# Kernel tuning notes

Measured on AMD Instinct MI355X. Metric: run time of the kernel, lower is better.

## Reference

```python
import jax, jax.numpy as jnp
import numpy as np

# Production-scale dims (see shape_source)
N = 100_000      # total nodes (tokens)
E = 1_600_000    # edges
B = 2_000        # graphs / documents
VOCAB = 50_000
NW = 256         # word_vec width == GraphConv out channels (args.nw)
ENC = 512        # args.enc_nh
K = 100          # args.num_topic
EPS = 1e-5       # BatchNorm eps


def setup_inputs() -> dict:
    key = jax.random.key(0)
    ks = jax.random.split(key, 24)
    idx_x = jax.random.randint(ks[0], (N,), 0, VOCAB)
    idx_w = jnp.ones((1,), jnp.float32)          # scalar self-loop weight
    x_batch = jnp.sort(jax.random.randint(ks[1], (N,), 0, B))
    edge_index = jax.random.randint(ks[2], (2, E), 0, N)
    edge_weight = jax.random.uniform(ks[3], (E,), jnp.float32)
    # Parameters
    s = 0.02
    word_vec = jax.random.normal(ks[4], (VOCAB, NW), jnp.float32) * s
    Wrel = jax.random.normal(ks[5], (NW, NW), jnp.float32) * s   # GraphConv lin_rel
    brel = jnp.zeros((NW,), jnp.float32)
    Wroot = jax.random.normal(ks[6], (NW, NW), jnp.float32) * s  # GraphConv lin_root (no bias)
    bn_gamma = jnp.ones((NW,), jnp.float32)
    bn_beta = jnp.zeros((NW,), jnp.float32)
    W1 = jax.random.normal(ks[7], (ENC, 2 * NW), jnp.float32) * s  # enc2_fc1
    b1 = jnp.zeros((ENC,), jnp.float32)
    W2 = jax.random.normal(ks[8], (ENC, 2 * NW), jnp.float32) * s  # enc2_fc2
    b2 = jnp.zeros((ENC,), jnp.float32)
    Wm = jax.random.normal(ks[9], (K, ENC), jnp.float32) * s       # mean_fc
    bm = jnp.zeros((K,), jnp.float32)
    Wv = jnp.zeros((K, ENC), jnp.float32)                          # logvar_fc zero-init
    bv = jnp.zeros((K,), jnp.float32)
    Wphi = jax.random.normal(ks[10], (K, 2 * NW + ENC), jnp.float32) * s  # phi_fc
    bphi = jnp.zeros((K,), jnp.float32)
    return dict(idx_x=idx_x, idx_w=idx_w, x_batch=x_batch, edge_index=edge_index,
                edge_weight=edge_weight, word_vec=word_vec, Wrel=Wrel, brel=brel,
                Wroot=Wroot, bn_gamma=bn_gamma, bn_beta=bn_beta, W1=W1, b1=b1,
                W2=W2, b2=b2, Wm=Wm, bm=bm, Wv=Wv, bv=bv, Wphi=Wphi, bphi=bphi)


def reference(idx_x, idx_w, x_batch, edge_index, edge_weight, word_vec,
              Wrel, brel, Wroot, bn_gamma, bn_beta, W1, b1, W2, b2,
              Wm, bm, Wv, bv, Wphi, bphi):
    # Embedding gather
    x = word_vec[idx_x]                                # [N, NW]
    src, dst = edge_index[0], edge_index[1]
    # GraphConv with explicit self-loops of weight idx_w (diag edges in original)
    msg = edge_weight[:, None] * x[src]                # [E, NW]
    aggr = jax.ops.segment_sum(msg, dst, num_segments=N) + idx_w * x
    h = aggr @ Wrel.T + brel + x @ Wroot.T             # lin_rel(aggr) + lin_root(x)
    # BatchNorm1d (training-mode batch stats, biased variance) + tanh
    mu = jnp.mean(h, axis=0)
    var = jnp.mean((h - mu) ** 2, axis=0)
    enc1 = jnp.tanh((h - mu) * jax.lax.rsqrt(var + EPS) * bn_gamma + bn_beta)
    enc1 = jnp.concatenate([enc1, x], axis=-1)         # [N, 2*NW]
    # GLU gate
    enc2 = jax.nn.sigmoid(enc1 @ W1.T + b1) * jnp.tanh(enc1 @ W2.T + b2)  # [N, ENC]
    # Scatter-sum pooling per document (dropout is identity in eval)
    pooled = jax.ops.segment_sum(enc2, x_batch, num_segments=B)            # [B, ENC]
    mean = pooled @ Wm.T + bm                          # [B, K]
    logvar = pooled @ Wv.T + bv                        # [B, K]
    # Gather re-expansion + softmax
    word_embed = jnp.concatenate([enc1, pooled[x_batch]], axis=-1)         # [N, 2*NW+ENC]
    phi = jax.nn.softmax(word_embed @ Wphi.T + bphi, axis=-1)              # [N, K]
    return mean, logvar, phi
```

## Files before the change

kernel.cpp:

```cpp
#include <hip/hip_runtime.h>
#include <hip/hip_bf16.h>

#define NW 256
#define D2 512
#define PK 1024
#define BM 128
#define BK 64
#define DPB 8

typedef unsigned short u16;
typedef short bf16x8 __attribute__((ext_vector_type(8)));
typedef float f32x4 __attribute__((ext_vector_type(4)));

__device__ __forceinline__ float bf2f(u16 u) {
    union { unsigned u; float f; } v; v.u = ((unsigned)u) << 16; return v.f;
}
__device__ __forceinline__ u16 f2bf(float f) {
    union { float f; unsigned u; } v; v.f = f;
    unsigned u = v.u;
    return (u16)((u + 0x7fffu + ((u >> 16) & 1u)) >> 16);
}
__device__ __forceinline__ float tanh_fast(float x) {
    return 1.f - 2.f / (1.f + __expf(2.f * x));
}

__device__ __forceinline__ void stage_tile(const u16* __restrict__ base, int row0, int maxrow,
                                           int ldk, int k0, u16* lds, int tid) {
    int w = tid >> 6, l = tid & 63;
#pragma unroll
    for (int i = 0; i < 4; ++i) {
        int loadIdx = i * 256 + w * 64 + l;
        int row = loadIdx >> 3, s = loadIdx & 7;
        int srow = row0 + row; if (srow > maxrow) srow = maxrow;
        int scol = k0 + ((s ^ (row & 7)) << 3);
        const u16* g = base + (size_t)srow * ldk + scol;
        u16* ld = lds + (size_t)(i * 256 + w * 64) * 8;
        __builtin_amdgcn_global_load_lds((const __attribute__((address_space(1))) void*)g,
                                         (__attribute__((address_space(3))) void*)ld, 16, 0, 0);
    }
}

__device__ __forceinline__ bf16x8 lds_frag(const u16* lds, int row, int kc, int g) {
    int byte = (row << 7) + (kc << 6) + (g << 4);
    byte ^= (row & 7) << 4;
    return *(const bf16x8*)((const char*)lds + byte);
}

__global__ void k_wcat(const float* __restrict__ Wrel, const float* __restrict__ Wroot,
                       u16* __restrict__ wcat) {
    int i = blockIdx.x * blockDim.x + threadIdx.x;
    if (i < NW * D2) {
        int c = i >> 9, k = i & 511;
        float v = (k < NW) ? Wrel[c * NW + k] : Wroot[c * NW + (k - NW)];
        wcat[i] = f2bf(v);
    }
}
__global__ void k_wpair(const float* __restrict__ W1, const float* __restrict__ W2,
                        u16* __restrict__ wp) {
    int i = blockIdx.x * blockDim.x + threadIdx.x;
    if (i < 1024 * 512) {
        int row = i >> 9, k = i & 511;
        int c = row >> 7, j = row & 127;
        float v = (j < 64) ? W1[(size_t)(c * 64 + j) * D2 + k]
                           : W2[(size_t)(c * 64 + j - 64) * D2 + k];
        wp[i] = f2bf(v);
    }
}
__global__ void k_wphi(const float* __restrict__ Wphi, u16* __restrict__ wp, int K) {
    int i = blockIdx.x * blockDim.x + threadIdx.x;
    if (i < 128 * 1024) {
        int r = i >> 10, k = i & 1023;
        wp[i] = f2bf(r < K ? Wphi[(size_t)r * PK + k] : 0.f);
    }
}

__global__ void k_gather(const int* __restrict__ idx, const float* __restrict__ wv,
                         u16* __restrict__ X, int N) {
    int row = blockIdx.x * 4 + (threadIdx.x >> 6);
    int lane = threadIdx.x & 63;
    if (row < N) {
        int id = idx[row];
        float4 v = *(const float4*)(wv + (size_t)id * NW + lane * 4);
        ushort4 o;
        o.x = f2bf(v.x); o.y = f2bf(v.y); o.z = f2bf(v.z); o.w = f2bf(v.w);
        *(ushort4*)(X + (size_t)row * D2 + NW + lane * 4) = o;
    }
}

__global__ void k_hist(const int* __restrict__ ei, int* __restrict__ deg, int E) {
    int e = blockIdx.x * blockDim.x + threadIdx.x;
    if (e < E) atomicAdd(&deg[ei[E + e]], 1);
}
__global__ __launch_bounds__(1024) void k_scan(const int* __restrict__ deg,
                                               int* __restrict__ rowptr, int N) {
    const int T = 1024;
    int t = threadIdx.x;
    int chunk = (N + T - 1) / T;
    int beg = t * chunk, end = min(beg + chunk, N);
    int s = 0;
    for (int i = beg; i < end; ++i) s += deg[i];
    __shared__ int ls[T];
    ls[t] = s; __syncthreads();
    for (int d = 1; d < T; d <<= 1) {
        int v = (t >= d) ? ls[t - d] : 0;
        __syncthreads();
        ls[t] += v;
        __syncthreads();
    }
    int run = ls[t] - s;
    for (int i = beg; i < end; ++i) { rowptr[i] = run; run += deg[i]; }
    if (t == T - 1) rowptr[N] = run;
}
__global__ void k_scatter(const int* __restrict__ ei, const float* __restrict__ ew,
                          const int* __restrict__ rowptr, int* __restrict__ cursor,
                          int* __restrict__ ecols, float* __restrict__ evals, int E) {
    int e = blockIdx.x * blockDim.x + threadIdx.x;
    if (e < E) {
        int d = ei[E + e];
        int p = rowptr[d] + atomicAdd(&cursor[d], 1);
        ecols[p] = ei[e];
        evals[p] = ew[e];
    }
}

__global__ void k_spmm(const int* __restrict__ rowptr, const int* __restrict__ ecols,
                       const float* __restrict__ evals, const float* __restrict__ idxw,
                       u16* __restrict__ X, int N) {
    int n = blockIdx.x * 4 + (threadIdx.x >> 6);
    int l = threadIdx.x & 63;
    if (n >= N) return;
    int half = l >> 5, li = l & 31;
    float a[8];
    bf16x8 xv = *(const bf16x8*)(X + (size_t)n * D2 + NW + li * 8);
    float iw = idxw[0];
#pragma unroll
    for (int j = 0; j < 8; ++j) a[j] = half ? 0.f : iw * bf2f((u16)xv[j]);
    int r0 = rowptr[n], r1 = rowptr[n + 1];
#pragma unroll 4
    for (int e = r0 + half; e < r1; e += 2) {
        int s = ecols[e];
        float w = evals[e];
        bf16x8 v = *(const bf16x8*)(X + (size_t)s * D2 + NW + li * 8);
#pragma unroll
        for (int j = 0; j < 8; ++j) a[j] += w * bf2f((u16)v[j]);
    }
#pragma unroll
    for (int j = 0; j < 8; ++j) a[j] += __shfl_xor(a[j], 32);
    if (half == 0) {
        bf16x8 o;
#pragma unroll
        for (int j = 0; j < 8; ++j) o[j] = (short)f2bf(a[j]);
        *(bf16x8*)(X + (size_t)n * D2 + li * 8) = o;
    }
}

__global__ __launch_bounds__(256) void k_gemm_h(const u16* __restrict__ A, const u16* __restrict__ W,
                                                const float* __restrict__ brel, u16* __restrict__ H,
                                                float* __restrict__ sums, float* __restrict__ sumsq,
                                                int M, int MT) {
    int b = blockIdx.x;
    int xcd = b & 7, j = b >> 3;
    int chunk = j & 1;
    int panel = (j >> 1) * 8 + xcd;
    if (panel >= MT) return;
    __shared__ u16 As[2][BM * BK], Ws[2][BM * BK];
    int tid = threadIdx.x;
    int w = tid >> 6, l = tid & 63, l16 = l & 15, g = l >> 4;
    int row0 = panel * BM;
    const u16* wbase = W + (size_t)chunk * 128 * D2;
    f32x4 acc[2][8];
#pragma unroll
    for (int m = 0; m < 2; ++m)
#pragma unroll
        for (int n = 0; n < 8; ++n) { f32x4 z = {0.f, 0.f, 0.f, 0.f}; acc[m][n] = z; }

    stage_tile(A, row0, M - 1, D2, 0, As[0], tid);
    stage_tile(wbase, 0, 127, D2, 0, Ws[0], tid);
    __syncthreads();
    int buf = 0;
    for (int kt = 0; kt < 8; ++kt) {
        if (kt < 7) {
            stage_tile(A, row0, M - 1, D2, (kt + 1) * BK, As[buf ^ 1], tid);
            stage_tile(wbase, 0, 127, D2, (kt + 1) * BK, Ws[buf ^ 1], tid);
        }
#pragma unroll
        for (int kc = 0; kc < 2; ++kc) {
            bf16x8 a0 = lds_frag(As[buf], w * 32 + l16, kc, g);
            bf16x8 a1 = lds_frag(As[buf], w * 32 + 16 + l16, kc, g);
#pragma unroll
            for (int n = 0; n < 8; ++n) {
                bf16x8 bb = lds_frag(Ws[buf], n * 16 + l16, kc, g);
                acc[0][n] = __builtin_amdgcn_mfma_f32_16x16x32_bf16(a0, bb, acc[0][n], 0, 0, 0);
                acc[1][n] = __builtin_amdgcn_mfma_f32_16x16x32_bf16(a1, bb, acc[1][n], 0, 0, 0);
            }
        }
        __syncthreads();
        buf ^= 1;
    }
    float* ssum = (float*)As[0];
    float* ssq  = ssum + 128;
    if (tid < 128) { ssum[tid] = 0.f; ssq[tid] = 0.f; }
    __syncthreads();
    int colb = chunk * 128;
#pragma unroll
    for (int n = 0; n < 8; ++n) {
        int lcol = n * 16 + l16;
        int col = colb + lcol;
        float bb = brel[col];
        float cs = 0.f, cq = 0.f;
#pragma unroll
        for (int m = 0; m < 2; ++m) {
            int row = row0 + w * 32 + m * 16 + g * 4;
#pragma unroll
            for (int r = 0; r < 4; ++r) {
                if (row + r < M) {
                    float v = acc[m][n][r] + bb;
                    H[(size_t)(row + r) * NW + col] = f2bf(v);
                    cs += v; cq += v * v;
                }
            }
        }
        cs += __shfl_xor(cs, 16); cs += __shfl_xor(cs, 32);
        cq += __shfl_xor(cq, 16); cq += __shfl_xor(cq, 32);
        if (g == 0) { atomicAdd(&ssum[lcol], cs); atomicAdd(&ssq[lcol], cq); }
    }
    __syncthreads();
    if (tid < 128) {
        atomicAdd(&sums[colb + tid], ssum[tid]);
        atomicAdd(&sumsq[colb + tid], ssq[tid]);
    }
}

__global__ void k_bnprep(const float* __restrict__ sums, const float* __restrict__ sumsq,
                         const float* __restrict__ gamma, const float* __restrict__ beta,
                         float* __restrict__ bnab, int N) {
    int c = threadIdx.x;
    float inv = 1.f / (float)N;
    float mu = sums[c] * inv;
    float var = sumsq[c] * inv - mu * mu;
    float rs = rsqrtf(var + 1e-5f);
    float a = rs * gamma[c];
    bnab[c] = a;
    bnab[NW + c] = beta[c] - mu * a;
}

__global__ void k_enc1(const u16* __restrict__ H, const float* __restrict__ bnab,
                       u16* __restrict__ X, int N) {
    int row = blockIdx.x * 4 + (threadIdx.x >> 6);
    int lane = threadIdx.x & 63;
    if (row >= N) return;
    int c = lane * 4;
    ushort4 hv = *(const ushort4*)(H + (size_t)row * NW + c);
    ushort4 o;
    o.x = f2bf(tanh_fast(bf2f(hv.x) * bnab[c + 0] + bnab[NW + c + 0]));
    o.y = f2bf(tanh_fast(bf2f(hv.y) * bnab[c + 1] + bnab[NW + c + 1]));
    o.z = f2bf(tanh_fast(bf2f(hv.z) * bnab[c + 2] + bnab[NW + c + 2]));
    o.w = f2bf(tanh_fast(bf2f(hv.w) * bnab[c + 3] + bnab[NW + c + 3]));
    *(ushort4*)(X + (size_t)row * D2 + c) = o;
}

__global__ __launch_bounds__(256) void k_glu(const u16* __restrict__ A, const u16* __restrict__ Wp,
                                             const float* __restrict__ b1, const float* __restrict__ b2,
                                             u16* __restrict__ enc2, int M, int MT) {
    int b = blockIdx.x;
    int xcd = b & 7, j = b >> 3;
    int chunk = j & 7;
    int panel = (j >> 3) * 8 + xcd;
    if (panel >= MT) return;
    __shared__ u16 As[2][BM * BK], Ws[2][BM * BK];
    int tid = threadIdx.x;
    int w = tid >> 6, l = tid & 63, l16 = l & 15, g = l >> 4;
    int row0 = panel * BM;
    const u16* wbase = Wp + (size_t)chunk * 128 * D2;
    f32x4 acc[2][8];
#pragma unroll
    for (int m = 0; m < 2; ++m)
#pragma unroll
        for (int n = 0; n < 8; ++n) { f32x4 z = {0.f, 0.f, 0.f, 0.f}; acc[m][n] = z; }

    stage_tile(A, row0, M - 1, D2, 0, As[0], tid);
    stage_tile(wbase, 0, 127, D2, 0, Ws[0], tid);
    __syncthreads();
    int buf = 0;
    for (int kt = 0; kt < 8; ++kt) {
        if (kt < 7) {
            stage_tile(A, row0, M - 1, D2, (kt + 1) * BK, As[buf ^ 1], tid);
            stage_tile(wbase, 0, 127, D2, (kt + 1) * BK, Ws[buf ^ 1], tid);
        }
#pragma unroll
        for (int kc = 0; kc < 2; ++kc) {
            bf16x8 a0 = lds_frag(As[buf], w * 32 + l16, kc, g);
            bf16x8 a1 = lds_frag(As[buf], w * 32 + 16 + l16, kc, g);
#pragma unroll
            for (int n = 0; n < 8; ++n) {
                bf16x8 bb = lds_frag(Ws[buf], n * 16 + l16, kc, g);
                acc[0][n] = __builtin_amdgcn_mfma_f32_16x16x32_bf16(a0, bb, acc[0][n], 0, 0, 0);
                acc[1][n] = __builtin_amdgcn_mfma_f32_16x16x32_bf16(a1, bb, acc[1][n], 0, 0, 0);
            }
        }
        __syncthreads();
        buf ^= 1;
    }
    int colb = chunk * 64;
#pragma unroll
    for (int m = 0; m < 2; ++m) {
        int row = row0 + w * 32 + m * 16 + g * 4;
#pragma unroll
        for (int n = 0; n < 4; ++n) {
            int col = colb + n * 16 + l16;
            float f1 = b1[col], f2 = b2[col];
#pragma unroll
            for (int r = 0; r < 4; ++r) {
                if (row + r < M) {
                    float g1 = acc[m][n][r] + f1;
                    float g2 = acc[m][n + 4][r] + f2;
                    float sg = 1.f / (1.f + __expf(-g1));
                    enc2[(size_t)(row + r) * D2 + col] = f2bf(sg * tanh_fast(g2));
                }
            }
        }
    }
}

__global__ void k_docptr(const int* __restrict__ xb, int* __restrict__ dp, int N, int B) {
    int b = blockIdx.x * blockDim.x + threadIdx.x;
    if (b <= B) {
        int lo = 0, hi = N;
        while (lo < hi) { int mid = (lo + hi) >> 1; if (xb[mid] < b) lo = mid + 1; else hi = mid; }
        dp[b] = lo;
    }
}

__global__ void k_pool(const u16* __restrict__ enc2, const int* __restrict__ dp,
                       float* __restrict__ pooled, u16* __restrict__ pooledb, int B) {
    int b = blockIdx.x, t = threadIdx.x;
    int r0 = dp[b], r1 = dp[b + 1];
    float a0 = 0.f, a1 = 0.f;
    for (int r = r0; r < r1; ++r) {
        a0 += bf2f(enc2[(size_t)r * D2 + t]);
        a1 += bf2f(enc2[(size_t)r * D2 + 256 + t]);
    }
    pooled[(size_t)b * D2 + t] = a0;
    pooled[(size_t)b * D2 + 256 + t] = a1;
    pooledb[(size_t)b * D2 + t] = f2bf(a0);
    pooledb[(size_t)b * D2 + 256 + t] = f2bf(a1);
}

__global__ __launch_bounds__(128) void k_meanvar(const float* __restrict__ pooled,
                                                 const float* __restrict__ Wm,
                                                 const float* __restrict__ bm,
                                                 const float* __restrict__ Wv,
                                                 const float* __restrict__ bv,
                                                 float* __restrict__ out, int B, int K) {
    __shared__ float sp[DPB][D2];
    int b0 = blockIdx.x * DPB;
    int t = threadIdx.x;
    for (int i = t; i < DPB * D2; i += 128) {
        int d = i >> 9, c = i & 511;
        int b = b0 + d;
        sp[d][c] = (b < B) ? pooled[(size_t)b * D2 + c] : 0.f;
    }
    __syncthreads();
    if (t < K) {
        float m[DPB], v[DPB];
#pragma unroll
        for (int d = 0; d < DPB; ++d) { m[d] = 0.f; v[d] = 0.f; }
        const float* wm = Wm + (size_t)t * D2;
        const float* wv = Wv + (size_t)t * D2;
        for (int c = 0; c < D2; ++c) {
            float a = wm[c], bb = wv[c];
#pragma unroll
            for (int d = 0; d < DPB; ++d) {
                m[d] += sp[d][c] * a;
                v[d] += sp[d][c] * bb;
            }
        }
        float mb = bm[t], vb = bv[t];
#pragma unroll
        for (int d = 0; d < DPB; ++d) {
            int b = b0 + d;
            if (b < B) {
                out[(size_t)b * K + t] = m[d] + mb;
                out[(size_t)B * K + (size_t)b * K + t] = v[d] + vb;
            }
        }
    }
}

__device__ __forceinline__ void stage_phiA(const u16* __restrict__ X, const u16* __restrict__ PB,
                                           const int* __restrict__ xb, int row0, int M,
                                           int k0, u16* lds, int tid) {
    int w = tid >> 6, l = tid & 63;
#pragma unroll
    for (int i = 0; i < 4; ++i) {
        int loadIdx = i * 256 + w * 64 + l;
        int row = loadIdx >> 3, s = loadIdx & 7;
        int srow = row0 + row; if (srow >= M) srow = M - 1;
        int scol = k0 + ((s ^ (row & 7)) << 3);
        const u16* gsrc = (scol < D2) ? X + (size_t)srow * D2 + scol
                                      : PB + (size_t)xb[srow] * D2 + (scol - D2);
        u16* ld = lds + (size_t)(i * 256 + w * 64) * 8;
        __builtin_amdgcn_global_load_lds((const __attribute__((address_space(1))) void*)gsrc,
                                         (__attribute__((address_space(3))) void*)ld, 16, 0, 0);
    }
}

__global__ __launch_bounds__(256) void k_phi(const u16* __restrict__ X, const u16* __restrict__ PB,
                                             const int* __restrict__ xb, const u16* __restrict__ Wp,
                                             const float* __restrict__ bphi, float* __restrict__ out,
                                             int M, int B, int K) {
    __shared__ u16 As[2][BM * BK], Ws[2][BM * BK];
    int tid = threadIdx.x;
    int w = tid >> 6, l = tid & 63, l16 = l & 15, g = l >> 4;
    int row0 = blockIdx.x * BM;
    f32x4 acc[2][8];
#pragma unroll
    for (int m = 0; m < 2; ++m)
#pragma unroll
        for (int n = 0; n < 8; ++n) { f32x4 z = {0.f, 0.f, 0.f, 0.f}; acc[m][n] = z; }

    stage_phiA(X, PB, xb, row0, M, 0, As[0], tid);
    stage_tile(Wp, 0, 127, PK, 0, Ws[0], tid);
    __syncthreads();
    int buf = 0;
    for (int kt = 0; kt < 16; ++kt) {
        if (kt < 15) {
            stage_phiA(X, PB, xb, row0, M, (kt + 1) * BK, As[buf ^ 1], tid);
            stage_tile(Wp, 0, 127, PK, (kt + 1) * BK, Ws[buf ^ 1], tid);
        }
#pragma unroll
        for (int kc = 0; kc < 2; ++kc) {
            bf16x8 a0 = lds_frag(As[buf], w * 32 + l16, kc, g);
            bf16x8 a1 = lds_frag(As[buf], w * 32 + 16 + l16, kc, g);
#pragma unroll
            for (int n = 0; n < 8; ++n) {
                bf16x8 bb = lds_frag(Ws[buf], n * 16 + l16, kc, g);
                acc[0][n] = __builtin_amdgcn_mfma_f32_16x16x32_bf16(a0, bb, acc[0][n], 0, 0, 0);
                acc[1][n] = __builtin_amdgcn_mfma_f32_16x16x32_bf16(a1, bb, acc[1][n], 0, 0, 0);
            }
        }
        __syncthreads();
        buf ^= 1;
    }
    size_t outoff = (size_t)2 * B * K;
#pragma unroll
    for (int m = 0; m < 2; ++m) {
        int rb = row0 + w * 32 + m * 16 + g * 4;
#pragma unroll
        for (int r = 0; r < 4; ++r) {
            int row = rb + r;
            if (row >= M) continue;
            float v[7];
            float mx = -1e30f;
#pragma unroll
            for (int n = 0; n < 7; ++n) {
                int col = n * 16 + l16;
                float t = (col < K) ? acc[m][n][r] + bphi[col] : -1e30f;
                v[n] = t;
                mx = fmaxf(mx, t);
            }
            mx = fmaxf(mx, __shfl_xor(mx, 1));
            mx = fmaxf(mx, __shfl_xor(mx, 2));
            mx = fmaxf(mx, __shfl_xor(mx, 4));
            mx = fmaxf(mx, __shfl_xor(mx, 8));
            float s = 0.f;
#pragma unroll
            for (int n = 0; n < 7; ++n) {
                int col = n * 16 + l16;
                float e = (col < K) ? __expf(v[n] - mx) : 0.f;
                v[n] = e;
                s += e;
            }
            s += __shfl_xor(s, 1);
            s += __shfl_xor(s, 2);
            s += __shfl_xor(s, 4);
            s += __shfl_xor(s, 8);
            float inv = 1.f / s;
#pragma unroll
            for (int n = 0; n < 7; ++n) {
                int col = n * 16 + l16;
                if (col < K) out[outoff + (size_t)row * K + col] = v[n] * inv;
            }
        }
    }
}

extern "C" void kernel_launch(void* const* d_in, const int* in_sizes, int n_in,
                              void* d_out, int out_size, void* d_ws, size_t ws_size,
                              hipStream_t stream) {
    const int N = in_sizes[0];
    const int E = in_sizes[4];
    const int K = in_sizes[16];
    const int B = (int)(((size_t)out_size - (size_t)N * K) / (2 * (size_t)K));

    const int*   idx_x   = (const int*)d_in[0];
    const float* idx_w   = (const float*)d_in[1];
    const int*   x_batch = (const int*)d_in[2];
    const int*   ei      = (const int*)d_in[3];
    const float* ew      = (const float*)d_in[4];
    const float* word_vec= (const float*)d_in[5];
    const float* Wrel    = (const float*)d_in[6];
    const float* brel    = (const float*)d_in[7];
    const float* Wroot   = (const float*)d_in[8];
    const float* gamma   = (const float*)d_in[9];
    const float* beta    = (const float*)d_in[10];
    const float* W1      = (const float*)d_in[11];
    const float* b1      = (const float*)d_in[12];
    const float* W2      = (const float*)d_in[13];
    const float* b2      = (const float*)d_in[14];
    const float* Wm      = (const float*)d_in[15];
    const float* bm      = (const float*)d_in[16];
    const float* Wv      = (const float*)d_in[17];
    const float* bv      = (const float*)d_in[18];
    const float* Wphi    = (const float*)d_in[19];
    const float* bphi    = (const float*)d_in[20];
    float* out = (float*)d_out;

    char* p = (char*)d_ws;
    auto take = [&](size_t bytes) -> char* {
        char* r = p;
        p += (bytes + 255) & ~(size_t)255;
        return r;
    };
    u16* X = (u16*)take((size_t)N * D2 * 2);
    char* Ybase = take((size_t)N * D2 * 2);
    u16*   hb   = (u16*)Ybase;
    u16*   enc2 = (u16*)Ybase;
    char* q = Ybase;
    auto takeY = [&](size_t bytes) -> char* {
        char* r = q;
        q += (bytes + 255) & ~(size_t)255;
        return r;
    };
    int*   rowptr = (int*)takeY((size_t)(N + 1) * 4);
    int*   cursor = (int*)takeY((size_t)N * 4);
    int*   ecols  = (int*)takeY((size_t)E * 4);
    float* evals  = (float*)takeY((size_t)E * 4);
    u16*   wcat    = (u16*)take((size_t)NW * D2 * 2);
    u16*   wglu    = (u16*)take((size_t)1024 * D2 * 2);
    u16*   wphib   = (u16*)take((size_t)128 * PK * 2);
    int*   docptr  = (int*)take((size_t)(B + 1) * 4);
    float* pooled  = (float*)take((size_t)B * D2 * 4);
    u16*   pooledb = (u16*)take((size_t)B * D2 * 2);
    float* sums    = (float*)take(NW * 4);
    float* sumsq   = (float*)take(NW * 4);
    float* bnab    = (float*)take(2 * NW * 4);

    if ((size_t)(p - (char*)d_ws) > ws_size) return;

    hipMemsetAsync(cursor, 0, (size_t)N * 4, stream);
    hipMemsetAsync(sums, 0, NW * 4, stream);
    hipMemsetAsync(sumsq, 0, NW * 4, stream);

    k_wcat<<<(NW * D2 + 255) / 256, 256, 0, stream>>>(Wrel, Wroot, wcat);
    k_wpair<<<(1024 * D2 + 255) / 256, 256, 0, stream>>>(W1, W2, wglu);
    k_wphi<<<(128 * PK + 255) / 256, 256, 0, stream>>>(Wphi, wphib, K);

    k_gather<<<(N + 3) / 4, 256, 0, stream>>>(idx_x, word_vec, X, N);
    k_hist<<<(E + 255) / 256, 256, 0, stream>>>(ei, cursor, E);
    k_scan<<<1, 1024, 0, stream>>>(cursor, rowptr, N);
    hipMemsetAsync(cursor, 0, (size_t)N * 4, stream);
    k_scatter<<<(E + 255) / 256, 256, 0, stream>>>(ei, ew, rowptr, cursor, ecols, evals, E);
    k_spmm<<<(N + 3) / 4, 256, 0, stream>>>(rowptr, ecols, evals, idx_w, X, N);

    int MT = (N + BM - 1) / BM;
    int P8 = (MT + 7) / 8;
    k_gemm_h<<<P8 * 8 * 2, 256, 0, stream>>>(X, wcat, brel, hb, sums, sumsq, N, MT);
    k_bnprep<<<1, NW, 0, stream>>>(sums, sumsq, gamma, beta, bnab, N);
    k_enc1<<<(N + 3) / 4, 256, 0, stream>>>(hb, bnab, X, N);

    k_glu<<<P8 * 8 * 8, 256, 0, stream>>>(X, wglu, b1, b2, enc2, N, MT);

    k_docptr<<<(B + 1 + 255) / 256, 256, 0, stream>>>(x_batch, docptr, N, B);
    k_pool<<<B, 256, 0, stream>>>(enc2, docptr, pooled, pooledb, B);
    k_meanvar<<<(B + DPB - 1) / DPB, 128, 0, stream>>>(pooled, Wm, bm, Wv, bv, out, B, K);
    k_phi<<<MT, 256, 0, stream>>>(X, pooledb, x_batch, wphib, bphi, out, N, B, K);
}
```

Baseline: 949.2 us.

## Use 2x2 wave tiling in GEMMs and merge weight prep and memsets

The h-GEMM and GLU GEMM kernels change from each wave owning 32 rows by 128 columns to a 2x2 wave grid where each wave owns 64x64. Per k-step this needs 8 LDS fragment loads per 16 MFMAs instead of 10, which lowers LDS traffic. The GLU weights are interleaved at 32-column granularity so each wave holds matching W1 and W2 columns. Separately, the three weight conversion kernels and two memsets are merged into one launch, and the scan now zeroes the degree counters itself, which removes another memset.

```diff
diff --git a/kernel.cpp b/kernel.cpp
--- a/kernel.cpp
+++ b/kernel.cpp
@@ -46,32 +46,32 @@
     return *(const bf16x8*)((const char*)lds + byte);
 }
 
-__global__ void k_wcat(const float* __restrict__ Wrel, const float* __restrict__ Wroot,
-                       u16* __restrict__ wcat) {
+__global__ void k_wprep(const float* __restrict__ Wrel, const float* __restrict__ Wroot,
+                        const float* __restrict__ W1, const float* __restrict__ W2,
+                        const float* __restrict__ Wphi,
+                        u16* __restrict__ wcat, u16* __restrict__ wglu,
+                        u16* __restrict__ wphib, float* __restrict__ sums,
+                        float* __restrict__ sumsq, int K) {
     int i = blockIdx.x * blockDim.x + threadIdx.x;
     if (i < NW * D2) {
         int c = i >> 9, k = i & 511;
         float v = (k < NW) ? Wrel[c * NW + k] : Wroot[c * NW + (k - NW)];
         wcat[i] = f2bf(v);
     }
-}
-__global__ void k_wpair(const float* __restrict__ W1, const float* __restrict__ W2,
-                        u16* __restrict__ wp) {
-    int i = blockIdx.x * blockDim.x + threadIdx.x;
     if (i < 1024 * 512) {
         int row = i >> 9, k = i & 511;
         int c = row >> 7, j = row & 127;
-        float v = (j < 64) ? W1[(size_t)(c * 64 + j) * D2 + k]
-                           : W2[(size_t)(c * 64 + j - 64) * D2 + k];
-        wp[i] = f2bf(v);
-    }
-}
-__global__ void k_wphi(const float* __restrict__ Wphi, u16* __restrict__ wp, int K) {
-    int i = blockIdx.x * blockDim.x + threadIdx.x;
+        int sub = j >> 5, jj = j & 31;
+        int half = sub & 1, colgrp = sub >> 1;
+        int col = c * 64 + colgrp * 32 + jj;
+        float v = half ? W2[(size_t)col * D2 + k] : W1[(size_t)col * D2 + k];
+        wglu[i] = f2bf(v);
+    }
     if (i < 128 * 1024) {
         int r = i >> 10, k = i & 1023;
-        wp[i] = f2bf(r < K ? Wphi[(size_t)r * PK + k] : 0.f);
-    }
+        wphib[i] = f2bf(r < K ? Wphi[(size_t)r * PK + k] : 0.f);
+    }
+    if (i < NW) { sums[i] = 0.f; sumsq[i] = 0.f; }
 }
 
 __global__ void k_gather(const int* __restrict__ idx, const float* __restrict__ wv,
@@ -91,7 +91,7 @@
     int e = blockIdx.x * blockDim.x + threadIdx.x;
     if (e < E) atomicAdd(&deg[ei[E + e]], 1);
 }
-__global__ __launch_bounds__(1024) void k_scan(const int* __restrict__ deg,
+__global__ __launch_bounds__(1024) void k_scan(int* __restrict__ deg,
                                                int* __restrict__ rowptr, int N) {
     const int T = 1024;
     int t = threadIdx.x;
@@ -108,7 +108,12 @@
         __syncthreads();
     }
     int run = ls[t] - s;
-    for (int i = beg; i < end; ++i) { rowptr[i] = run; run += deg[i]; }
+    for (int i = beg; i < end; ++i) {
+        int d = deg[i];
+        rowptr[i] = run;
+        run += d;
+        deg[i] = 0;
+    }
     if (t == T - 1) rowptr[N] = run;
 }
 __global__ void k_scatter(const int* __restrict__ ei, const float* __restrict__ ew,
@@ -166,13 +171,14 @@
     __shared__ u16 As[2][BM * BK], Ws[2][BM * BK];
     int tid = threadIdx.x;
     int w = tid >> 6, l = tid & 63, l16 = l & 15, g = l >> 4;
+    int wr = w >> 1, wc = w & 1;
     int row0 = panel * BM;
     const u16* wbase = W + (size_t)chunk * 128 * D2;
-    f32x4 acc[2][8];
-#pragma unroll
-    for (int m = 0; m < 2; ++m)
-#pragma unroll
-        for (int n = 0; n < 8; ++n) { f32x4 z = {0.f, 0.f, 0.f, 0.f}; acc[m][n] = z; }
+    f32x4 acc[4][4];
+#pragma unroll
+    for (int m = 0; m < 4; ++m)
+#pragma unroll
+        for (int n = 0; n < 4; ++n) { f32x4 z = {0.f, 0.f, 0.f, 0.f}; acc[m][n] = z; }
 
     stage_tile(A, row0, M - 1, D2, 0, As[0], tid);
     stage_tile(wbase, 0, 127, D2, 0, Ws[0], tid);
@@ -185,14 +191,16 @@
         }
 #pragma unroll
         for (int kc = 0; kc < 2; ++kc) {
-            bf16x8 a0 = lds_frag(As[buf], w * 32 + l16, kc, g);
-            bf16x8 a1 = lds_frag(As[buf], w * 32 + 16 + l16, kc, g);
-#pragma unroll
-            for (int n = 0; n < 8; ++n) {
-                bf16x8 bb = lds_frag(Ws[buf], n * 16 + l16, kc, g);
-                acc[0][n] = __builtin_amdgcn_mfma_f32_16x16x32_bf16(a0, bb, acc[0][n], 0, 0, 0);
-                acc[1][n] = __builtin_amdgcn_mfma_f32_16x16x32_bf16(a1, bb, acc[1][n], 0, 0, 0);
-            }
+            bf16x8 af[4], bfr[4];
+#pragma unroll
+            for (int m = 0; m < 4; ++m) af[m] = lds_frag(As[buf], wr * 64 + m * 16 + l16, kc, g);
+#pragma unroll
+            for (int n = 0; n < 4; ++n) bfr[n] = lds_frag(Ws[buf], wc * 64 + n * 16 + l16, kc, g);
+#pragma unroll
+            for (int n = 0; n < 4; ++n)
+#pragma unroll
+                for (int m = 0; m < 4; ++m)
+                    acc[m][n] = __builtin_amdgcn_mfma_f32_16x16x32_bf16(af[m], bfr[n], acc[m][n], 0, 0, 0);
         }
         __syncthreads();
         buf ^= 1;
@@ -203,14 +211,14 @@
     __syncthreads();
     int colb = chunk * 128;
 #pragma unroll
-    for (int n = 0; n < 8; ++n) {
-        int lcol = n * 16 + l16;
+    for (int n = 0; n < 4; ++n) {
+        int lcol = wc * 64 + n * 16 + l16;
         int col = colb + lcol;
         float bb = brel[col];
         float cs = 0.f, cq = 0.f;
 #pragma unroll
-        for (int m = 0; m < 2; ++m) {
-            int row = row0 + w * 32 + m * 16 + g * 4;
+        for (int m = 0; m < 4; ++m) {
+            int row = row0 + wr * 64 + m * 16 + g * 4;
 #pragma unroll
             for (int r = 0; r < 4; ++r) {
                 if (row + r < M) {
@@ -270,13 +278,14 @@
     __shared__ u16 As[2][BM * BK], Ws[2][BM * BK];
     int tid = threadIdx.x;
     int w = tid >> 6, l = tid & 63, l16 = l & 15, g = l >> 4;
+    int wr = w >> 1, wc = w & 1;
     int row0 = panel * BM;
     const u16* wbase = Wp + (size_t)chunk * 128 * D2;
-    f32x4 acc[2][8];
-#pragma unroll
-    for (int m = 0; m < 2; ++m)
-#pragma unroll
-        for (int n = 0; n < 8; ++n) { f32x4 z = {0.f, 0.f, 0.f, 0.f}; acc[m][n] = z; }
+    f32x4 acc[4][4];
+#pragma unroll
+    for (int m = 0; m < 4; ++m)
+#pragma unroll
+        for (int n = 0; n < 4; ++n) { f32x4 z = {0.f, 0.f, 0.f, 0.f}; acc[m][n] = z; }
 
     stage_tile(A, row0, M - 1, D2, 0, As[0], tid);
     stage_tile(wbase, 0, 127, D2, 0, Ws[0], tid);
@@ -289,31 +298,33 @@
         }
 #pragma unroll
         for (int kc = 0; kc < 2; ++kc) {
-            bf16x8 a0 = lds_frag(As[buf], w * 32 + l16, kc, g);
-            bf16x8 a1 = lds_frag(As[buf], w * 32 + 16 + l16, kc, g);
-#pragma unroll
-            for (int n = 0; n < 8; ++n) {
-                bf16x8 bb = lds_frag(Ws[buf], n * 16 + l16, kc, g);
-                acc[0][n] = __builtin_amdgcn_mfma_f32_16x16x32_bf16(a0, bb, acc[0][n], 0, 0, 0);
-                acc[1][n] = __builtin_amdgcn_mfma_f32_16x16x32_bf16(a1, bb, acc[1][n], 0, 0, 0);
-            }
+            bf16x8 af[4], bfr[4];
+#pragma unroll
+            for (int m = 0; m < 4; ++m) af[m] = lds_frag(As[buf], wr * 64 + m * 16 + l16, kc, g);
+#pragma unroll
+            for (int n = 0; n < 4; ++n) bfr[n] = lds_frag(Ws[buf], wc * 64 + n * 16 + l16, kc, g);
+#pragma unroll
+            for (int n = 0; n < 4; ++n)
+#pragma unroll
+                for (int m = 0; m < 4; ++m)
+                    acc[m][n] = __builtin_amdgcn_mfma_f32_16x16x32_bf16(af[m], bfr[n], acc[m][n], 0, 0, 0);
         }
         __syncthreads();
         buf ^= 1;
     }
-    int colb = chunk * 64;
-#pragma unroll
-    for (int m = 0; m < 2; ++m) {
-        int row = row0 + w * 32 + m * 16 + g * 4;
-#pragma unroll
-        for (int n = 0; n < 4; ++n) {
-            int col = colb + n * 16 + l16;
-            float f1 = b1[col], f2 = b2[col];
+    int colb = chunk * 64 + wc * 32;
+#pragma unroll
+    for (int n = 0; n < 2; ++n) {
+        int col = colb + n * 16 + l16;
+        float f1 = b1[col], f2 = b2[col];
+#pragma unroll
+        for (int m = 0; m < 4; ++m) {
+            int row = row0 + wr * 64 + m * 16 + g * 4;
 #pragma unroll
             for (int r = 0; r < 4; ++r) {
                 if (row + r < M) {
                     float g1 = acc[m][n][r] + f1;
-                    float g2 = acc[m][n + 4][r] + f2;
+                    float g2 = acc[m][n + 2][r] + f2;
                     float sg = 1.f / (1.f + __expf(-g1));
                     enc2[(size_t)(row + r) * D2 + col] = f2bf(sg * tanh_fast(g2));
                 }
@@ -549,17 +560,13 @@
     if ((size_t)(p - (char*)d_ws) > ws_size) return;
 
     hipMemsetAsync(cursor, 0, (size_t)N * 4, stream);
-    hipMemsetAsync(sums, 0, NW * 4, stream);
-    hipMemsetAsync(sumsq, 0, NW * 4, stream);
-
-    k_wcat<<<(NW * D2 + 255) / 256, 256, 0, stream>>>(Wrel, Wroot, wcat);
-    k_wpair<<<(1024 * D2 + 255) / 256, 256, 0, stream>>>(W1, W2, wglu);
-    k_wphi<<<(128 * PK + 255) / 256, 256, 0, stream>>>(Wphi, wphib, K);
+
+    k_wprep<<<(1024 * 512 + 255) / 256, 256, 0, stream>>>(Wrel, Wroot, W1, W2, Wphi,
+                                                          wcat, wglu, wphib, sums, sumsq, K);
 
     k_gather<<<(N + 3) / 4, 256, 0, stream>>>(idx_x, word_vec, X, N);
     k_hist<<<(E + 255) / 256, 256, 0, stream>>>(ei, cursor, E);
     k_scan<<<1, 1024, 0, stream>>>(cursor, rowptr, N);
-    hipMemsetAsync(cursor, 0, (size_t)N * 4, stream);
     k_scatter<<<(E + 255) / 256, 256, 0, stream>>>(ei, ew, rowptr, cursor, ecols, evals, E);
     k_spmm<<<(N + 3) / 4, 256, 0, stream>>>(rowptr, ecols, evals, idx_w, X, N);
 
```

After: 984.5 us. +3.7%, slower.
